# Optimization experiments

Hardware: AMD Instinct MI355X
Metric: run time of the kernel (lower is better)

Reference implementation:

```python
import jax, jax.numpy as jnp
import numpy as np
from jax import lax

TOP_K = 4
ROUTED_SCALING = 1.0
RENORMALIZE = True


def setup_inputs() -> dict:
    key = jax.random.key(0)
    ks = jax.random.split(key, 9)
    H, I, E = 2048, 1024, 16
    s = 0.02
    return {
        "hidden_states": jax.random.normal(ks[0], (2, 1024, H), jnp.float32),
        "gate_w": jax.random.normal(ks[1], (E, H), jnp.float32) * s,
        "expert_bias": jax.random.normal(ks[2], (E,), jnp.float32) * s,
        "w_gate": jax.random.normal(ks[3], (E, I, H), jnp.float32) * s,
        "w_up": jax.random.normal(ks[4], (E, I, H), jnp.float32) * s,
        "w_down": jax.random.normal(ks[5], (E, H, I), jnp.float32) * s,
        "sw_gate": jax.random.normal(ks[6], (I, H), jnp.float32) * s,
        "sw_up": jax.random.normal(ks[7], (I, H), jnp.float32) * s,
        "sw_down": jax.random.normal(ks[8], (H, I), jnp.float32) * s,
    }


def _swiglu_ffn(x, wg, wu, wd):
    # SiluAndMul(gate_up) -> down_proj
    return (jax.nn.silu(x @ wg.T) * (x @ wu.T)) @ wd.T


def reference(hidden_states, gate_w, expert_bias, w_gate, w_up, w_down,
              sw_gate, sw_up, sw_down):
    orig_shape = hidden_states.shape
    H = orig_shape[-1]
    x = hidden_states.reshape(-1, H)            # [T, H]
    T = x.shape[0]

    # --- sigmoid gating with score-correction bias (bias affects selection only) ---
    logits = x.astype(jnp.float32) @ gate_w.T    # [T, E] fp32 router
    scores = jax.nn.sigmoid(logits)
    _, topk_idx = lax.top_k(scores + expert_bias[None, :], TOP_K)   # [T, K]
    topk_w = jnp.take_along_axis(scores, topk_idx, axis=-1)         # raw scores
    if RENORMALIZE:
        topk_w = topk_w / jnp.sum(topk_w, axis=-1, keepdims=True)
    topk_w = topk_w * ROUTED_SCALING

    # scatter top-k weights into dense [T, E] combine matrix
    E = gate_w.shape[0]
    combine = jnp.zeros((T, E), dtype=x.dtype).at[
        jnp.arange(T)[:, None], topk_idx].set(topk_w.astype(x.dtype))

    # --- routed experts: scan over experts, weighted accumulate ---
    def step(acc, ws):
        wg, wu, wd, cw = ws                     # cw: [T] combine weights
        return acc + cw[:, None] * _swiglu_ffn(x, wg, wu, wd), None

    routed, _ = lax.scan(step, jnp.zeros_like(x),
                         (w_gate, w_up, w_down, combine.T))

    # --- shared expert ---
    shared = _swiglu_ffn(x, sw_gate, sw_up, sw_down)

    return (routed + shared).reshape(orig_shape)
```

## Files before the change

kernel.cpp:

```cpp
#include <hip/hip_runtime.h>
#include <hip/hip_bf16.h>
#include <cstdint>

#define TK 2048
#define HD 2048
#define ID 1024
#define NE 16
#define NG 17
#define TOPK 4
#define SLOTS (TK*TOPK)
#define ROWS_ALL (SLOTS+TK)
#define IH (ID*HD)
#define MAXT 96

typedef __attribute__((ext_vector_type(4))) float f32x4;
typedef __attribute__((ext_vector_type(16))) float f32x16;
typedef __attribute__((ext_vector_type(8))) short s16x8;
typedef unsigned short u16;
typedef unsigned long long u64;

__device__ __forceinline__ u16 f2bf(float f){
  union { float f; uint32_t u; } v; v.f = f;
  uint32_t r = v.u + 0x7fffu + ((v.u >> 16) & 1u);
  return (u16)(r >> 16);
}

#define GLD16(g, l) __builtin_amdgcn_global_load_lds( \
    (const __attribute__((address_space(1))) void*)(g), \
    (__attribute__((address_space(3))) void*)(l), 16, 0, 0)

__device__ __forceinline__ int swz(int r){
  return (r & 7) ^ (((r >> 3) & 3) << 1);
}
__device__ __forceinline__ const s16x8* fragp(const u16* b, int row, int off){
  return (const s16x8*)((const char*)b + row*128 + (off ^ (swz(row)<<4)));
}

#define MFMA32(a,b,c) __builtin_amdgcn_mfma_f32_32x32x16_bf16((a),(b),(c),0,0,0)

__global__ void k_prep(const float* __restrict__ x, u16* __restrict__ xb,
                       u64* __restrict__ maskbits, int* __restrict__ tokcnt){
  int gi = blockIdx.x*blockDim.x + threadIdx.x;
  int st = gridDim.x*blockDim.x;
  if (gi < NE*32) maskbits[gi] = 0ull;
  if (gi < TK) tokcnt[gi] = 0;
  for (int i=gi; i<TK*HD/4; i+=st){
    float4 f = ((const float4*)x)[i];
    ushort4 o; o.x=f2bf(f.x); o.y=f2bf(f.y); o.z=f2bf(f.z); o.w=f2bf(f.w);
    ((ushort4*)xb)[i] = o;
  }
}

__global__ void k_cvtw(const float* __restrict__ wg, const float* __restrict__ wu,
                       const float* __restrict__ wd, const float* __restrict__ swg,
                       const float* __restrict__ swu, const float* __restrict__ swd,
                       u16* __restrict__ wgb, u16* __restrict__ wub, u16* __restrict__ wdb){
  const size_t nbig = (size_t)NE*IH/4, nsml = IH/4;
  const size_t total = 3*nbig + 3*nsml;
  for (size_t i = (size_t)blockIdx.x*blockDim.x + threadIdx.x; i < total;
       i += (size_t)gridDim.x*blockDim.x){
    const float4* src; ushort4* dst; size_t j = i;
    if (j < nbig){ src=(const float4*)wg + j;  dst=(ushort4*)wgb + j; }
    else if ((j-=nbig) < nbig){ src=(const float4*)wu + j;  dst=(ushort4*)wub + j; }
    else if ((j-=nbig) < nbig){ src=(const float4*)wd + j;  dst=(ushort4*)wdb + j; }
    else if ((j-=nbig) < nsml){ src=(const float4*)swg + j; dst=(ushort4*)wgb + nbig + j; }
    else if ((j-=nsml) < nsml){ src=(const float4*)swu + j; dst=(ushort4*)wub + nbig + j; }
    else { j-=nsml; src=(const float4*)swd + j; dst=(ushort4*)wdb + nbig + j; }
    float4 f = *src;
    ushort4 o; o.x=f2bf(f.x); o.y=f2bf(f.y); o.z=f2bf(f.z); o.w=f2bf(f.w);
    *dst = o;
  }
}

__global__ __launch_bounds__(256) void k_logits(const float* __restrict__ x,
                                                const float* __restrict__ gw,
                                                const float* __restrict__ bias,
                                                float* __restrict__ wdense,
                                                u64* __restrict__ maskbits){
  int t = blockIdx.x, tid = threadIdx.x;
  int lane = tid & 63, wv = tid >> 6;
  const float* xr = x + (size_t)t*HD;
  float acc[NE];
  #pragma unroll
  for (int e=0;e<NE;e++) acc[e]=0.f;
  for (int k=tid;k<HD;k+=256){
    float xv = xr[k];
    #pragma unroll
    for (int e=0;e<NE;e++) acc[e] += xv * gw[e*HD + k];
  }
  __shared__ float red[NE][4];
  #pragma unroll
  for (int e=0;e<NE;e++){
    float v = acc[e];
    #pragma unroll
    for (int off=32;off>0;off>>=1) v += __shfl_down(v, off, 64);
    if (lane==0) red[e][wv] = v;
  }
  __syncthreads();
  if (tid == 0){
    float sc[NE], bs[NE];
    #pragma unroll
    for (int e=0;e<NE;e++){
      float l = red[e][0]+red[e][1]+red[e][2]+red[e][3];
      float s = 1.f/(1.f+expf(-l));
      sc[e]=s; bs[e]=s+bias[e];
    }
    int idx[TOPK]; float wsum=0.f; unsigned used=0;
    for (int k=0;k<TOPK;k++){
      int best=0; float bv=-1e30f;
      for (int e=0;e<NE;e++) if (!((used>>e)&1u) && bs[e] > bv){ bv=bs[e]; best=e; }
      used |= 1u<<best; idx[k]=best; wsum += sc[best];
    }
    float inv = 1.f/wsum;
    for (int k=0;k<TOPK;k++){
      int e = idx[k];
      wdense[t*NE + e] = sc[e]*inv;
      atomicOr(&maskbits[e*32 + (t>>6)], 1ull << (t&63));
    }
  }
}

__global__ void k_scan(const u64* __restrict__ maskbits, int* __restrict__ counts,
                       int* __restrict__ offsets, int* __restrict__ wordpfx,
                       int* __restrict__ tiles){
  int acc = 0;
  for (int e=0;e<NE;e++){
    int c = 0;
    for (int w=0;w<32;w++){ wordpfx[e*32+w] = c; c += __popcll(maskbits[e*32+w]); }
    counts[e] = c;
  }
  for (int e=0;e<NE;e++){ offsets[e] = acc; acc += counts[e]; }
  offsets[NE] = acc;
  counts[NE] = TK;
  int nt = 0;
  for (int g=0; g<NG; g++){
    int c = counts[g];
    for (int mt=0; mt*128 < c && nt < MAXT; mt++) tiles[nt++] = (g<<8) | mt;
  }
  for (; nt<MAXT; nt++) tiles[nt] = -1;
}

__global__ void k_scatter(const u64* __restrict__ maskbits, const int* __restrict__ offsets,
                          const int* __restrict__ wordpfx, const float* __restrict__ wdense,
                          int* __restrict__ rowtok, float* __restrict__ roww,
                          int* __restrict__ tokcnt, int* __restrict__ tok4){
  int t = blockIdx.x*blockDim.x + threadIdx.x;
  int e = blockIdx.y;
  if (t >= TK) return;
  if (e == NE){ rowtok[offsets[NE]+t] = t; roww[offsets[NE]+t] = 1.f; return; }
  u64 w = maskbits[e*32 + (t>>6)];
  if ((w >> (t&63)) & 1ull){
    int pos = offsets[e] + wordpfx[e*32 + (t>>6)] + __popcll(w & ((1ull << (t&63)) - 1ull));
    rowtok[pos] = t; roww[pos] = wdense[t*NE + e];
    int r = atomicAdd(&tokcnt[t], 1);
    tok4[t*TOPK + r] = pos;
  }
}

__global__ __launch_bounds__(256, 2) void k_gemm1b(
    const u16* __restrict__ xb, const u16* __restrict__ wgb, const u16* __restrict__ wub,
    const int* __restrict__ counts, const int* __restrict__ offsets,
    const int* __restrict__ rowtok, const float* __restrict__ roww,
    const int* __restrict__ tiles, u16* __restrict__ P)
{
  int te = tiles[blockIdx.y];
  if (te < 0) return;
  int g = te >> 8, mt = te & 255;
  int cnt = counts[g];
  int n0 = blockIdx.x*128;
  int base = offsets[g];
  const u16* wg16 = wgb + (size_t)g*IH;
  const u16* wu16 = wub + (size_t)g*IH;

  __shared__ u16 lsA[128*64];
  __shared__ u16 lsG[128*64];
  __shared__ u16 lsU[128*64];

  int tid = threadIdx.x, lane = tid & 63, wv = tid >> 6;
  int wm = (wv>>1)*64, wn64 = (wv&1)*64;
  int rl = lane & 31, hi = lane >> 5;

  f32x16 accg[2][2] = {}; f32x16 accu[2][2] = {};

  const u16 *aSrc[4], *gSrc[4], *uSrc[4];
  #pragma unroll
  for (int i=0;i<4;i++){
    int b = i*256 + tid, r = b>>3, cb = b&7;
    int m = mt*128 + r; if (m >= cnt) m = cnt-1;
    int tok = rowtok[base + m];
    aSrc[i] = xb + (size_t)tok*HD + ((cb ^ swz(r))<<3);
    size_t woff = (size_t)(n0 + r)*HD + ((cb ^ swz(r))<<3);
    gSrc[i] = wg16 + woff; uSrc[i] = wu16 + woff;
  }

  for (int t=0; t<HD/64; ++t){
    int k0 = t*64;
    #pragma unroll
    for (int i=0;i<4;i++) GLD16(aSrc[i]+k0, lsA + (i*256 + wv*64)*8);
    #pragma unroll
    for (int i=0;i<4;i++) GLD16(gSrc[i]+k0, lsG + (i*256 + wv*64)*8);
    #pragma unroll
    for (int i=0;i<4;i++) GLD16(uSrc[i]+k0, lsU + (i*256 + wv*64)*8);
    asm volatile("s_waitcnt vmcnt(0)" ::: "memory");
    __builtin_amdgcn_s_barrier();
    #pragma unroll
    for (int s=0; s<4; ++s){
      int off = s*32 + hi*16;
      s16x8 af[2], bg[2], bu[2];
      af[0] = *fragp(lsA, wm + rl, off);
      af[1] = *fragp(lsA, wm + 32 + rl, off);
      bg[0] = *fragp(lsG, wn64 + rl, off);
      bg[1] = *fragp(lsG, wn64 + 32 + rl, off);
      bu[0] = *fragp(lsU, wn64 + rl, off);
      bu[1] = *fragp(lsU, wn64 + 32 + rl, off);
      #pragma unroll
      for (int mi=0;mi<2;mi++){
        #pragma unroll
        for (int j=0;j<2;j++){
          accg[mi][j] = MFMA32(af[mi], bg[j], accg[mi][j]);
          accu[mi][j] = MFMA32(af[mi], bu[j], accu[mi][j]);
        }
      }
    }
    asm volatile("s_waitcnt lgkmcnt(0)" ::: "memory");
    __builtin_amdgcn_s_barrier();
  }
  #pragma unroll
  for (int mi=0;mi<2;mi++){
    #pragma unroll
    for (int r=0;r<16;r++){
      int rowb = wm + mi*32 + (r&3) + 8*(r>>2) + 4*hi;
      int m = mt*128 + rowb;
      if (m < cnt){
        int slot = base + m;
        float wgt = roww[slot];
        #pragma unroll
        for (int j=0;j<2;j++){
          float gv = accg[mi][j][r], uv = accu[mi][j][r];
          float pv = gv/(1.f+expf(-gv))*uv*wgt;
          P[(size_t)slot*ID + n0 + wn64 + j*32 + rl] = f2bf(pv);
        }
      }
    }
  }
}

__global__ __launch_bounds__(256, 2) void k_gemm2b(
    const u16* __restrict__ P, const u16* __restrict__ wdb,
    const int* __restrict__ counts, const int* __restrict__ offsets,
    const int* __restrict__ tiles, u16* __restrict__ R)
{
  int te = tiles[blockIdx.y];
  if (te < 0) return;
  int g = te >> 8, mt = te & 255;
  int cnt = counts[g];
  int base = offsets[g];
  int n0 = blockIdx.x*256;
  const u16* wd16 = wdb + (size_t)g*IH;

  __shared__ u16 lsA[128*64];
  __shared__ u16 lsB[256*64];

  int tid = threadIdx.x, lane = tid & 63, wv = tid >> 6;
  int wm = (wv>>1)*64, wn = (wv&1)*128;
  int rl = lane & 31, hi = lane >> 5;
  f32x16 acc[2][4] = {};

  const u16* aSrc[4];
  #pragma unroll
  for (int i=0;i<4;i++){
    int b = i*256 + tid, r = b>>3, cb = b&7;
    int m = mt*128 + r; if (m >= cnt) m = cnt-1;
    aSrc[i] = P + (size_t)(base + m)*ID + ((cb ^ swz(r))<<3);
  }
  const u16* bSrc[8];
  #pragma unroll
  for (int i=0;i<8;i++){
    int b = i*256 + tid, r = b>>3, cb = b&7;
    bSrc[i] = wd16 + (size_t)(n0 + r)*ID + ((cb ^ swz(r))<<3);
  }

  for (int t=0; t<ID/64; ++t){
    int k0 = t*64;
    #pragma unroll
    for (int i=0;i<4;i++) GLD16(aSrc[i]+k0, lsA + (i*256 + wv*64)*8);
    #pragma unroll
    for (int i=0;i<8;i++) GLD16(bSrc[i]+k0, lsB + (i*256 + wv*64)*8);
    asm volatile("s_waitcnt vmcnt(0)" ::: "memory");
    __builtin_amdgcn_s_barrier();
    #pragma unroll
    for (int s=0; s<4; ++s){
      int off = s*32 + hi*16;
      s16x8 af[2], bf[4];
      af[0] = *fragp(lsA, wm + rl, off);
      af[1] = *fragp(lsA, wm + 32 + rl, off);
      #pragma unroll
      for (int nj=0;nj<4;nj++) bf[nj] = *fragp(lsB, wn + nj*32 + rl, off);
      #pragma unroll
      for (int mi=0;mi<2;mi++)
        #pragma unroll
        for (int nj=0;nj<4;nj++)
          acc[mi][nj] = MFMA32(af[mi], bf[nj], acc[mi][nj]);
    }
    asm volatile("s_waitcnt lgkmcnt(0)" ::: "memory");
    __builtin_amdgcn_s_barrier();
  }
  #pragma unroll
  for (int mi=0;mi<2;mi++){
    #pragma unroll
    for (int r=0;r<16;r++){
      int rowb = wm + mi*32 + (r&3) + 8*(r>>2) + 4*hi;
      int m = mt*128 + rowb;
      if (m < cnt){
        u16* rrow = R + (size_t)(base + m)*HD + n0 + wn + rl;
        #pragma unroll
        for (int nj=0;nj<4;nj++) rrow[nj*32] = f2bf(acc[mi][nj][r]);
      }
    }
  }
}

__global__ __launch_bounds__(256) void k_reduce(const u16* __restrict__ R,
                                                const int* __restrict__ tok4,
                                                float* __restrict__ out){
  int t = blockIdx.x;
  int c0 = threadIdx.x * 8;
  int s0 = tok4[t*TOPK+0], s1 = tok4[t*TOPK+1], s2 = tok4[t*TOPK+2], s3 = tok4[t*TOPK+3];
  const ushort4* p0 = (const ushort4*)(R + (size_t)s0*HD + c0);
  const ushort4* p1 = (const ushort4*)(R + (size_t)s1*HD + c0);
  const ushort4* p2 = (const ushort4*)(R + (size_t)s2*HD + c0);
  const ushort4* p3 = (const ushort4*)(R + (size_t)s3*HD + c0);
  const ushort4* ps = (const ushort4*)(R + (size_t)(SLOTS + t)*HD + c0);
  float* o = out + (size_t)t*HD + c0;
  #pragma unroll
  for (int h=0; h<2; h++){
    ushort4 a = p0[h], b = p1[h], c = p2[h], d = p3[h], e = ps[h];
    #pragma unroll
    for (int j=0;j<4;j++){
      u16 ua = ((const u16*)&a)[j], ub = ((const u16*)&b)[j];
      u16 uc = ((const u16*)&c)[j], ud = ((const u16*)&d)[j], ue = ((const u16*)&e)[j];
      float v = ((float)(int)0);
      union { uint32_t u; float f; } w;
      w.u = (uint32_t)ua<<16; v  = w.f;
      w.u = (uint32_t)ub<<16; v += w.f;
      w.u = (uint32_t)uc<<16; v += w.f;
      w.u = (uint32_t)ud<<16; v += w.f;
      w.u = (uint32_t)ue<<16; v += w.f;
      o[h*4 + j] = v;
    }
  }
}


extern "C" void kernel_launch(void* const* d_in, const int* in_sizes, int n_in,
                              void* d_out, int out_size, void* d_ws, size_t ws_size,
                              hipStream_t stream){
  (void)in_sizes; (void)n_in; (void)ws_size; (void)out_size;
  const float* x       = (const float*)d_in[0];
  const float* gate_w  = (const float*)d_in[1];
  const float* ebias   = (const float*)d_in[2];
  const float* w_gate  = (const float*)d_in[3];
  const float* w_up    = (const float*)d_in[4];
  const float* w_down  = (const float*)d_in[5];
  const float* sw_gate = (const float*)d_in[6];
  const float* sw_up   = (const float*)d_in[7];
  const float* sw_down = (const float*)d_in[8];
  float* out = (float*)d_out;

  char* p = (char*)d_ws;
  auto alloc = [&](size_t bytes)->char*{ char* r = p; p += (bytes + 255) & ~(size_t)255; return r; };
  u16*   xb       = (u16*)  alloc((size_t)TK*HD*2);
  u16*   P        = (u16*)  alloc((size_t)ROWS_ALL*ID*2);
  float* wdense   = (float*)alloc((size_t)TK*NE*4);
  u64*   maskbits = (u64*)  alloc((size_t)NE*32*8);
  int*   wordpfx  = (int*)  alloc((size_t)NE*32*4);
  int*   counts   = (int*)  alloc(64);
  int*   offsets  = (int*)  alloc(64);
  int*   tiles    = (int*)  alloc(MAXT*4);
  int*   rowtok   = (int*)  alloc((size_t)ROWS_ALL*4);
  float* roww     = (float*)alloc((size_t)ROWS_ALL*4);
  int*   tokcnt   = (int*)  alloc((size_t)TK*4);
  int*   tok4     = (int*)  alloc((size_t)TK*TOPK*4);
  size_t slab = (size_t)NG*IH*2;
  u16* wgb = (u16*)alloc(slab);
  u16* wub = (u16*)alloc(slab);
  u16* wdb = (u16*)alloc(slab);
  u16* R = wgb;

  k_prep<<<2048, 256, 0, stream>>>(x, xb, maskbits, tokcnt);
  k_cvtw<<<2048, 256, 0, stream>>>(w_gate, w_up, w_down, sw_gate, sw_up, sw_down,
                                   wgb, wub, wdb);
  k_logits<<<TK, 256, 0, stream>>>(x, gate_w, ebias, wdense, maskbits);
  k_scan<<<1, 1, 0, stream>>>(maskbits, counts, offsets, wordpfx, tiles);
  k_scatter<<<dim3(TK/256, NG), 256, 0, stream>>>(maskbits, offsets, wordpfx, wdense,
                                                  rowtok, roww, tokcnt, tok4);

  dim3 g1(ID/128, MAXT);
  k_gemm1b<<<g1, 256, 0, stream>>>(xb, wgb, wub, counts, offsets, rowtok, roww, tiles, P);
  dim3 g2(HD/256, MAXT);
  k_gemm2b<<<g2, 256, 0, stream>>>(P, wdb, counts, offsets, tiles, R);
  k_reduce<<<TK, 256, 0, stream>>>(R, tok4, out);
}
```

Before: 393.2 us.

## Interleave gate/up weights, enlarge GEMM tiles to 256x256, double-buffer LDS

Weight conversion now interleaves gate and up rows in blocks of 32 into one buffer, so gemm1 loads a single B tile and computes gate/up pairs within each wave. Both grouped GEMMs move to 512-thread blocks with 256-row M tiles and 256-column N tiles, and they double-buffer LDS with prefetch of the next K slice and raised wave priority around the MFMA loop. The swizzle is simplified to row&7 and the tile count per expert is halved. The aim is more data reuse per block and load latency hidden behind compute. The cost is larger LDS use (128KB) and more padding waste for experts with small token counts.

Measured after the change: 422.8 us. 7.5% more time.

```diff
diff --git a/kernel.cpp b/kernel.cpp
--- a/kernel.cpp
+++ b/kernel.cpp
@@ -11,7 +11,7 @@
 #define SLOTS (TK*TOPK)
 #define ROWS_ALL (SLOTS+TK)
 #define IH (ID*HD)
-#define MAXT 96
+#define MAXT 64
 
 typedef __attribute__((ext_vector_type(4))) float f32x4;
 typedef __attribute__((ext_vector_type(16))) float f32x16;
@@ -29,11 +29,8 @@
     (const __attribute__((address_space(1))) void*)(g), \
     (__attribute__((address_space(3))) void*)(l), 16, 0, 0)
 
-__device__ __forceinline__ int swz(int r){
-  return (r & 7) ^ (((r >> 3) & 3) << 1);
-}
 __device__ __forceinline__ const s16x8* fragp(const u16* b, int row, int off){
-  return (const s16x8*)((const char*)b + row*128 + (off ^ (swz(row)<<4)));
+  return (const s16x8*)((const char*)b + row*128 + (off ^ ((row&7)<<4)));
 }
 
 #define MFMA32(a,b,c) __builtin_amdgcn_mfma_f32_32x32x16_bf16((a),(b),(c),0,0,0)
@@ -54,18 +51,34 @@
 __global__ void k_cvtw(const float* __restrict__ wg, const float* __restrict__ wu,
                        const float* __restrict__ wd, const float* __restrict__ swg,
                        const float* __restrict__ swu, const float* __restrict__ swd,
-                       u16* __restrict__ wgb, u16* __restrict__ wub, u16* __restrict__ wdb){
-  const size_t nbig = (size_t)NE*IH/4, nsml = IH/4;
-  const size_t total = 3*nbig + 3*nsml;
-  for (size_t i = (size_t)blockIdx.x*blockDim.x + threadIdx.x; i < total;
+                       u16* __restrict__ wgu, u16* __restrict__ wdb){
+  const size_t ngu = (size_t)NG*2048*(HD/4);
+  const size_t nd  = (size_t)NG*2048*(ID/4);
+  for (size_t i = (size_t)blockIdx.x*blockDim.x + threadIdx.x; i < ngu + nd;
        i += (size_t)gridDim.x*blockDim.x){
-    const float4* src; ushort4* dst; size_t j = i;
-    if (j < nbig){ src=(const float4*)wg + j;  dst=(ushort4*)wgb + j; }
-    else if ((j-=nbig) < nbig){ src=(const float4*)wu + j;  dst=(ushort4*)wub + j; }
-    else if ((j-=nbig) < nbig){ src=(const float4*)wd + j;  dst=(ushort4*)wdb + j; }
-    else if ((j-=nbig) < nsml){ src=(const float4*)swg + j; dst=(ushort4*)wgb + nbig + j; }
-    else if ((j-=nsml) < nsml){ src=(const float4*)swu + j; dst=(ushort4*)wub + nbig + j; }
-    else { j-=nsml; src=(const float4*)swd + j; dst=(ushort4*)wdb + nbig + j; }
+    const float4* src; ushort4* dst;
+    if (i < ngu){
+      int g   = (int)(i / (2048*(size_t)(HD/4)));
+      int rem = (int)(i % (2048*(size_t)(HD/4)));
+      int J   = rem / (HD/4);
+      int kv  = rem % (HD/4);
+      int rp  = (J>>6)*32 + (J&31);
+      const float* s;
+      if (g < NE) s = ((J&32) ? wu : wg) + (size_t)g*IH + (size_t)rp*HD;
+      else        s = ((J&32) ? swu : swg) + (size_t)rp*HD;
+      src = (const float4*)s + kv;
+      dst = (ushort4*)(wgu + (size_t)g*2048*HD + (size_t)J*HD) + kv;
+    } else {
+      size_t j = i - ngu;
+      int g   = (int)(j / (2048*(size_t)(ID/4)));
+      int rem = (int)(j % (2048*(size_t)(ID/4)));
+      int J   = rem / (ID/4);
+      int kv  = rem % (ID/4);
+      const float* s = (g < NE) ? (wd + (size_t)g*IH + (size_t)J*ID)
+                                : (swd + (size_t)J*ID);
+      src = (const float4*)s + kv;
+      dst = (ushort4*)(wdb + (size_t)g*2048*ID + (size_t)J*ID) + kv;
+    }
     float4 f = *src;
     ushort4 o; o.x=f2bf(f.x); o.y=f2bf(f.y); o.z=f2bf(f.z); o.w=f2bf(f.w);
     *dst = o;
@@ -135,7 +148,7 @@
   int nt = 0;
   for (int g=0; g<NG; g++){
     int c = counts[g];
-    for (int mt=0; mt*128 < c && nt < MAXT; mt++) tiles[nt++] = (g<<8) | mt;
+    for (int mt=0; mt*256 < c && nt < MAXT; mt++) tiles[nt++] = (g<<8) | mt;
   }
   for (; nt<MAXT; nt++) tiles[nt] = -1;
 }
@@ -157,8 +170,8 @@
   }
 }
 
-__global__ __launch_bounds__(256, 2) void k_gemm1b(
-    const u16* __restrict__ xb, const u16* __restrict__ wgb, const u16* __restrict__ wub,
+__global__ __launch_bounds__(512, 2) void k_gemm1b(
+    const u16* __restrict__ xb, const u16* __restrict__ wgu,
     const int* __restrict__ counts, const int* __restrict__ offsets,
     const int* __restrict__ rowtok, const float* __restrict__ roww,
     const int* __restrict__ tiles, u16* __restrict__ P)
@@ -167,85 +180,87 @@
   if (te < 0) return;
   int g = te >> 8, mt = te & 255;
   int cnt = counts[g];
-  int n0 = blockIdx.x*128;
+  int x = blockIdx.x;
   int base = offsets[g];
-  const u16* wg16 = wgb + (size_t)g*IH;
-  const u16* wu16 = wub + (size_t)g*IH;
-
-  __shared__ u16 lsA[128*64];
-  __shared__ u16 lsG[128*64];
-  __shared__ u16 lsU[128*64];
+  const u16* B0 = wgu + (size_t)g*2048*HD + (size_t)(x*256)*HD;
+
+  __shared__ u16 lsA[2][256*64];
+  __shared__ u16 lsB[2][256*64];
 
   int tid = threadIdx.x, lane = tid & 63, wv = tid >> 6;
-  int wm = (wv>>1)*64, wn64 = (wv&1)*64;
+  int wm = (wv>>2)*128, wc = wv & 3;
   int rl = lane & 31, hi = lane >> 5;
 
-  f32x16 accg[2][2] = {}; f32x16 accu[2][2] = {};
-
-  const u16 *aSrc[4], *gSrc[4], *uSrc[4];
+  f32x16 acc[4][2] = {};
+
+  const u16 *aSrc[4], *bSrc[4];
   #pragma unroll
   for (int i=0;i<4;i++){
-    int b = i*256 + tid, r = b>>3, cb = b&7;
-    int m = mt*128 + r; if (m >= cnt) m = cnt-1;
+    int c = i*512 + tid, r = c>>3, cb = c&7;
+    int m = mt*256 + r; if (m >= cnt) m = cnt-1;
     int tok = rowtok[base + m];
-    aSrc[i] = xb + (size_t)tok*HD + ((cb ^ swz(r))<<3);
-    size_t woff = (size_t)(n0 + r)*HD + ((cb ^ swz(r))<<3);
-    gSrc[i] = wg16 + woff; uSrc[i] = wu16 + woff;
-  }
-
-  for (int t=0; t<HD/64; ++t){
-    int k0 = t*64;
-    #pragma unroll
-    for (int i=0;i<4;i++) GLD16(aSrc[i]+k0, lsA + (i*256 + wv*64)*8);
-    #pragma unroll
-    for (int i=0;i<4;i++) GLD16(gSrc[i]+k0, lsG + (i*256 + wv*64)*8);
-    #pragma unroll
-    for (int i=0;i<4;i++) GLD16(uSrc[i]+k0, lsU + (i*256 + wv*64)*8);
-    asm volatile("s_waitcnt vmcnt(0)" ::: "memory");
+    aSrc[i] = xb + (size_t)tok*HD + ((cb ^ (r&7))<<3);
+    bSrc[i] = B0 + (size_t)r*HD + ((cb ^ (r&7))<<3);
+  }
+
+  #pragma unroll
+  for (int i=0;i<4;i++) GLD16(aSrc[i], &lsA[0][(i*512 + wv*64)*8]);
+  #pragma unroll
+  for (int i=0;i<4;i++) GLD16(bSrc[i], &lsB[0][(i*512 + wv*64)*8]);
+
+  const int ntile = HD/64;
+  for (int t=0; t<ntile; ++t){
+    int cur = t & 1, nxt = cur ^ 1;
+    if (t+1 < ntile){
+      int k1 = (t+1)*64;
+      #pragma unroll
+      for (int i=0;i<4;i++) GLD16(aSrc[i]+k1, &lsA[nxt][(i*512 + wv*64)*8]);
+      #pragma unroll
+      for (int i=0;i<4;i++) GLD16(bSrc[i]+k1, &lsB[nxt][(i*512 + wv*64)*8]);
+      asm volatile("s_waitcnt vmcnt(8)" ::: "memory");
+    } else {
+      asm volatile("s_waitcnt vmcnt(0)" ::: "memory");
+    }
     __builtin_amdgcn_s_barrier();
+    const u16* A = lsA[cur]; const u16* B = lsB[cur];
+    __builtin_amdgcn_s_setprio(1);
     #pragma unroll
     for (int s=0; s<4; ++s){
       int off = s*32 + hi*16;
-      s16x8 af[2], bg[2], bu[2];
-      af[0] = *fragp(lsA, wm + rl, off);
-      af[1] = *fragp(lsA, wm + 32 + rl, off);
-      bg[0] = *fragp(lsG, wn64 + rl, off);
-      bg[1] = *fragp(lsG, wn64 + 32 + rl, off);
-      bu[0] = *fragp(lsU, wn64 + rl, off);
-      bu[1] = *fragp(lsU, wn64 + 32 + rl, off);
-      #pragma unroll
-      for (int mi=0;mi<2;mi++){
-        #pragma unroll
-        for (int j=0;j<2;j++){
-          accg[mi][j] = MFMA32(af[mi], bg[j], accg[mi][j]);
-          accu[mi][j] = MFMA32(af[mi], bu[j], accu[mi][j]);
-        }
+      s16x8 af[4], bf[2];
+      #pragma unroll
+      for (int mi=0;mi<4;mi++) af[mi] = *fragp(A, wm + mi*32 + rl, off);
+      bf[0] = *fragp(B, wc*64 + rl, off);
+      bf[1] = *fragp(B, wc*64 + 32 + rl, off);
+      #pragma unroll
+      for (int mi=0;mi<4;mi++){
+        acc[mi][0] = MFMA32(af[mi], bf[0], acc[mi][0]);
+        acc[mi][1] = MFMA32(af[mi], bf[1], acc[mi][1]);
       }
     }
+    __builtin_amdgcn_s_setprio(0);
     asm volatile("s_waitcnt lgkmcnt(0)" ::: "memory");
     __builtin_amdgcn_s_barrier();
   }
-  #pragma unroll
-  for (int mi=0;mi<2;mi++){
+  int pcol = x*128 + wc*32 + rl;
+  #pragma unroll
+  for (int mi=0;mi<4;mi++){
     #pragma unroll
     for (int r=0;r<16;r++){
       int rowb = wm + mi*32 + (r&3) + 8*(r>>2) + 4*hi;
-      int m = mt*128 + rowb;
+      int m = mt*256 + rowb;
       if (m < cnt){
         int slot = base + m;
         float wgt = roww[slot];
-        #pragma unroll
-        for (int j=0;j<2;j++){
-          float gv = accg[mi][j][r], uv = accu[mi][j][r];
-          float pv = gv/(1.f+expf(-gv))*uv*wgt;
-          P[(size_t)slot*ID + n0 + wn64 + j*32 + rl] = f2bf(pv);
-        }
+        float gv = acc[mi][0][r], uv = acc[mi][1][r];
+        float pv = gv/(1.f+expf(-gv))*uv*wgt;
+        P[(size_t)slot*ID + pcol] = f2bf(pv);
       }
     }
   }
 }
 
-__global__ __launch_bounds__(256, 2) void k_gemm2b(
+__global__ __launch_bounds__(512, 2) void k_gemm2b(
     const u16* __restrict__ P, const u16* __restrict__ wdb,
     const int* __restrict__ counts, const int* __restrict__ offsets,
     const int* __restrict__ tiles, u16* __restrict__ R)
@@ -255,66 +270,76 @@
   int g = te >> 8, mt = te & 255;
   int cnt = counts[g];
   int base = offsets[g];
-  int n0 = blockIdx.x*256;
-  const u16* wd16 = wdb + (size_t)g*IH;
-
-  __shared__ u16 lsA[128*64];
-  __shared__ u16 lsB[256*64];
+  int x = blockIdx.x;
+  const u16* B0 = wdb + (size_t)g*2048*ID + (size_t)(x*256)*ID;
+
+  __shared__ u16 lsA[2][256*64];
+  __shared__ u16 lsB[2][256*64];
 
   int tid = threadIdx.x, lane = tid & 63, wv = tid >> 6;
-  int wm = (wv>>1)*64, wn = (wv&1)*128;
+  int wm = (wv>>2)*128, wc = wv & 3;
   int rl = lane & 31, hi = lane >> 5;
-  f32x16 acc[2][4] = {};
-
-  const u16* aSrc[4];
+  f32x16 acc[4][2] = {};
+
+  const u16 *aSrc[4], *bSrc[4];
   #pragma unroll
   for (int i=0;i<4;i++){
-    int b = i*256 + tid, r = b>>3, cb = b&7;
-    int m = mt*128 + r; if (m >= cnt) m = cnt-1;
-    aSrc[i] = P + (size_t)(base + m)*ID + ((cb ^ swz(r))<<3);
-  }
-  const u16* bSrc[8];
-  #pragma unroll
-  for (int i=0;i<8;i++){
-    int b = i*256 + tid, r = b>>3, cb = b&7;
-    bSrc[i] = wd16 + (size_t)(n0 + r)*ID + ((cb ^ swz(r))<<3);
-  }
-
-  for (int t=0; t<ID/64; ++t){
-    int k0 = t*64;
-    #pragma unroll
-    for (int i=0;i<4;i++) GLD16(aSrc[i]+k0, lsA + (i*256 + wv*64)*8);
-    #pragma unroll
-    for (int i=0;i<8;i++) GLD16(bSrc[i]+k0, lsB + (i*256 + wv*64)*8);
-    asm volatile("s_waitcnt vmcnt(0)" ::: "memory");
+    int c = i*512 + tid, r = c>>3, cb = c&7;
+    int m = mt*256 + r; if (m >= cnt) m = cnt-1;
+    aSrc[i] = P + (size_t)(base + m)*ID + ((cb ^ (r&7))<<3);
+    bSrc[i] = B0 + (size_t)r*ID + ((cb ^ (r&7))<<3);
+  }
+
+  #pragma unroll
+  for (int i=0;i<4;i++) GLD16(aSrc[i], &lsA[0][(i*512 + wv*64)*8]);
+  #pragma unroll
+  for (int i=0;i<4;i++) GLD16(bSrc[i], &lsB[0][(i*512 + wv*64)*8]);
+
+  const int ntile = ID/64;
+  for (int t=0; t<ntile; ++t){
+    int cur = t & 1, nxt = cur ^ 1;
+    if (t+1 < ntile){
+      int k1 = (t+1)*64;
+      #pragma unroll
+      for (int i=0;i<4;i++) GLD16(aSrc[i]+k1, &lsA[nxt][(i*512 + wv*64)*8]);
+      #pragma unroll
+      for (int i=0;i<4;i++) GLD16(bSrc[i]+k1, &lsB[nxt][(i*512 + wv*64)*8]);
+      asm volatile("s_waitcnt vmcnt(8)" ::: "memory");
+    } else {
+      asm volatile("s_waitcnt vmcnt(0)" ::: "memory");
+    }
     __builtin_amdgcn_s_barrier();
+    const u16* A = lsA[cur]; const u16* B = lsB[cur];
+    __builtin_amdgcn_s_setprio(1);
     #pragma unroll
     for (int s=0; s<4; ++s){
       int off = s*32 + hi*16;
-      s16x8 af[2], bf[4];
-      af[0] = *fragp(lsA, wm + rl, off);
-      af[1] = *fragp(lsA, wm + 32 + rl, off);
-      #pragma unroll
-      for (int nj=0;nj<4;nj++) bf[nj] = *fragp(lsB, wn + nj*32 + rl, off);
-      #pragma unroll
-      for (int mi=0;mi<2;mi++)
-        #pragma unroll
-        for (int nj=0;nj<4;nj++)
-          acc[mi][nj] = MFMA32(af[mi], bf[nj], acc[mi][nj]);
-    }
+      s16x8 af[4], bf[2];
+      #pragma unroll
+      for (int mi=0;mi<4;mi++) af[mi] = *fragp(A, wm + mi*32 + rl, off);
+      bf[0] = *fragp(B, wc*64 + rl, off);
+      bf[1] = *fragp(B, wc*64 + 32 + rl, off);
+      #pragma unroll
+      for (int mi=0;mi<4;mi++){
+        acc[mi][0] = MFMA32(af[mi], bf[0], acc[mi][0]);
+        acc[mi][1] = MFMA32(af[mi], bf[1], acc[mi][1]);
+      }
+    }
+    __builtin_amdgcn_s_setprio(0);
     asm volatile("s_waitcnt lgkmcnt(0)" ::: "memory");
     __builtin_amdgcn_s_barrier();
   }
   #pragma unroll
-  for (int mi=0;mi<2;mi++){
+  for (int mi=0;mi<4;mi++){
     #pragma unroll
     for (int r=0;r<16;r++){
       int rowb = wm + mi*32 + (r&3) + 8*(r>>2) + 4*hi;
-      int m = mt*128 + rowb;
+      int m = mt*256 + rowb;
       if (m < cnt){
-        u16* rrow = R + (size_t)(base + m)*HD + n0 + wn + rl;
-        #pragma unroll
-        for (int nj=0;nj<4;nj++) rrow[nj*32] = f2bf(acc[mi][nj][r]);
+        int slot = base + m;
+        u16* rrow = R + (size_t)slot*HD + x*256 + wc*64 + rl;
+        rrow[0]  = f2bf(acc[mi][0][r]);
+        rrow[32] = f2bf(acc[mi][1][r]);
       }
     }
   }
@@ -339,8 +364,8 @@
     for (int j=0;j<4;j++){
       u16 ua = ((const u16*)&a)[j], ub = ((const u16*)&b)[j];
       u16 uc = ((const u16*)&c)[j], ud = ((const u16*)&d)[j], ue = ((const u16*)&e)[j];
-      float v = ((float)(int)0);
       union { uint32_t u; float f; } w;
+      float v;
       w.u = (uint32_t)ua<<16; v  = w.f;
       w.u = (uint32_t)ub<<16; v += w.f;
       w.u = (uint32_t)uc<<16; v += w.f;
@@ -381,23 +406,21 @@
   float* roww     = (float*)alloc((size_t)ROWS_ALL*4);
   int*   tokcnt   = (int*)  alloc((size_t)TK*4);
   int*   tok4     = (int*)  alloc((size_t)TK*TOPK*4);
-  size_t slab = (size_t)NG*IH*2;
-  u16* wgb = (u16*)alloc(slab);
-  u16* wub = (u16*)alloc(slab);
-  u16* wdb = (u16*)alloc(slab);
-  u16* R = wgb;
+  u16* wgu = (u16*)alloc((size_t)NG*2048*HD*2);
+  u16* wdb = (u16*)alloc((size_t)NG*2048*ID*2);
+  u16* R = wgu;
 
   k_prep<<<2048, 256, 0, stream>>>(x, xb, maskbits, tokcnt);
   k_cvtw<<<2048, 256, 0, stream>>>(w_gate, w_up, w_down, sw_gate, sw_up, sw_down,
-                                   wgb, wub, wdb);
+                                   wgu, wdb);
   k_logits<<<TK, 256, 0, stream>>>(x, gate_w, ebias, wdense, maskbits);
   k_scan<<<1, 1, 0, stream>>>(maskbits, counts, offsets, wordpfx, tiles);
   k_scatter<<<dim3(TK/256, NG), 256, 0, stream>>>(maskbits, offsets, wordpfx, wdense,
                                                   rowtok, roww, tokcnt, tok4);
 
   dim3 g1(ID/128, MAXT);
-  k_gemm1b<<<g1, 256, 0, stream>>>(xb, wgb, wub, counts, offsets, rowtok, roww, tiles, P);
+  k_gemm1b<<<g1, 512, 0, stream>>>(xb, wgu, counts, offsets, rowtok, roww, tiles, P);
   dim3 g2(HD/256, MAXT);
-  k_gemm2b<<<g2, 256, 0, stream>>>(P, wdb, counts, offsets, tiles, R);
+  k_gemm2b<<<g2, 512, 0, stream>>>(P, wdb, counts, offsets, tiles, R);
   k_reduce<<<TK, 256, 0, stream>>>(R, tok4, out);
 }
```

## Switch grouped GEMMs to 16x16x32 MFMA with narrower gate/up N tile

Applied to the files above, without the earlier changes.

Both grouped expert GEMMs move from 32x32x16 to 16x16x32 bf16 MFMA instructions, which changes the fragment layouts, the accumulator shapes and the epilogue row mapping. The LDS swizzle is simplified to a plain row&7 XOR. The gate/up GEMM N tile is halved to 64, which doubles its grid in x and halves its LDS footprint. The second launch_bounds occupancy hint is dropped, so the compiler may use more registers, especially in gemm2 where the accumulator tile is larger. The aim is better occupancy and parallelism for gemm1, at the cost of rereading the A tile twice as often and of possible LDS bank conflicts from the weaker swizzle.

After: 425.9 us. 1.08x slower.

```diff
diff --git a/kernel.cpp b/kernel.cpp
--- a/kernel.cpp
+++ b/kernel.cpp
@@ -14,7 +14,6 @@
 #define MAXT 96
 
 typedef __attribute__((ext_vector_type(4))) float f32x4;
-typedef __attribute__((ext_vector_type(16))) float f32x16;
 typedef __attribute__((ext_vector_type(8))) short s16x8;
 typedef unsigned short u16;
 typedef unsigned long long u64;
@@ -29,14 +28,11 @@
     (const __attribute__((address_space(1))) void*)(g), \
     (__attribute__((address_space(3))) void*)(l), 16, 0, 0)
 
-__device__ __forceinline__ int swz(int r){
-  return (r & 7) ^ (((r >> 3) & 3) << 1);
-}
 __device__ __forceinline__ const s16x8* fragp(const u16* b, int row, int off){
-  return (const s16x8*)((const char*)b + row*128 + (off ^ (swz(row)<<4)));
-}
-
-#define MFMA32(a,b,c) __builtin_amdgcn_mfma_f32_32x32x16_bf16((a),(b),(c),0,0,0)
+  return (const s16x8*)((const char*)b + row*128 + (off ^ ((row&7)<<4)));
+}
+
+#define MFMA16(a,b,c) __builtin_amdgcn_mfma_f32_16x16x32_bf16((a),(b),(c),0,0,0)
 
 __global__ void k_prep(const float* __restrict__ x, u16* __restrict__ xb,
                        u64* __restrict__ maskbits, int* __restrict__ tokcnt){
@@ -157,7 +153,7 @@
   }
 }
 
-__global__ __launch_bounds__(256, 2) void k_gemm1b(
+__global__ __launch_bounds__(256) void k_gemm1b(
     const u16* __restrict__ xb, const u16* __restrict__ wgb, const u16* __restrict__ wub,
     const int* __restrict__ counts, const int* __restrict__ offsets,
     const int* __restrict__ rowtok, const float* __restrict__ roww,
@@ -167,85 +163,85 @@
   if (te < 0) return;
   int g = te >> 8, mt = te & 255;
   int cnt = counts[g];
-  int n0 = blockIdx.x*128;
+  int n0 = blockIdx.x*64;
   int base = offsets[g];
   const u16* wg16 = wgb + (size_t)g*IH;
   const u16* wu16 = wub + (size_t)g*IH;
 
   __shared__ u16 lsA[128*64];
-  __shared__ u16 lsG[128*64];
-  __shared__ u16 lsU[128*64];
+  __shared__ u16 lsG[64*64];
+  __shared__ u16 lsU[64*64];
 
   int tid = threadIdx.x, lane = tid & 63, wv = tid >> 6;
-  int wm = (wv>>1)*64, wn64 = (wv&1)*64;
-  int rl = lane & 31, hi = lane >> 5;
-
-  f32x16 accg[2][2] = {}; f32x16 accu[2][2] = {};
-
-  const u16 *aSrc[4], *gSrc[4], *uSrc[4];
+  int wm = (wv>>1)*64, wn = (wv&1)*32;
+  int rl = lane & 15, hi = lane >> 4;
+
+  f32x4 accg[4][2] = {}; f32x4 accu[4][2] = {};
+
+  const u16* aSrc[4];
   #pragma unroll
   for (int i=0;i<4;i++){
     int b = i*256 + tid, r = b>>3, cb = b&7;
     int m = mt*128 + r; if (m >= cnt) m = cnt-1;
     int tok = rowtok[base + m];
-    aSrc[i] = xb + (size_t)tok*HD + ((cb ^ swz(r))<<3);
-    size_t woff = (size_t)(n0 + r)*HD + ((cb ^ swz(r))<<3);
-    gSrc[i] = wg16 + woff; uSrc[i] = wu16 + woff;
-  }
-
-  for (int t=0; t<HD/64; ++t){
-    int k0 = t*64;
+    aSrc[i] = xb + (size_t)tok*HD + ((cb ^ (r&7))<<3);
+  }
+  const u16 *gSrc[2], *uSrc[2];
+  #pragma unroll
+  for (int i=0;i<2;i++){
+    int b = i*256 + tid, r = b>>3, cb = b&7;
+    size_t off = (size_t)(n0 + r)*HD + ((cb ^ (r&7))<<3);
+    gSrc[i] = wg16 + off; uSrc[i] = wu16 + off;
+  }
+
+  for (int k0=0; k0<HD; k0+=64){
     #pragma unroll
     for (int i=0;i<4;i++) GLD16(aSrc[i]+k0, lsA + (i*256 + wv*64)*8);
     #pragma unroll
-    for (int i=0;i<4;i++) GLD16(gSrc[i]+k0, lsG + (i*256 + wv*64)*8);
-    #pragma unroll
-    for (int i=0;i<4;i++) GLD16(uSrc[i]+k0, lsU + (i*256 + wv*64)*8);
-    asm volatile("s_waitcnt vmcnt(0)" ::: "memory");
-    __builtin_amdgcn_s_barrier();
-    #pragma unroll
-    for (int s=0; s<4; ++s){
-      int off = s*32 + hi*16;
-      s16x8 af[2], bg[2], bu[2];
-      af[0] = *fragp(lsA, wm + rl, off);
-      af[1] = *fragp(lsA, wm + 32 + rl, off);
-      bg[0] = *fragp(lsG, wn64 + rl, off);
-      bg[1] = *fragp(lsG, wn64 + 32 + rl, off);
-      bu[0] = *fragp(lsU, wn64 + rl, off);
-      bu[1] = *fragp(lsU, wn64 + 32 + rl, off);
-      #pragma unroll
-      for (int mi=0;mi<2;mi++){
+    for (int i=0;i<2;i++) GLD16(gSrc[i]+k0, lsG + (i*256 + wv*64)*8);
+    #pragma unroll
+    for (int i=0;i<2;i++) GLD16(uSrc[i]+k0, lsU + (i*256 + wv*64)*8);
+    __syncthreads();
+    #pragma unroll
+    for (int ks=0; ks<2; ++ks){
+      int off = ks*64 + hi*16;
+      s16x8 af[4];
+      #pragma unroll
+      for (int mi=0;mi<4;mi++) af[mi] = *fragp(lsA, wm+16*mi+rl, off);
+      #pragma unroll
+      for (int ni=0;ni<2;ni++){
+        s16x8 bg = *fragp(lsG, wn+16*ni+rl, off);
+        s16x8 bu = *fragp(lsU, wn+16*ni+rl, off);
         #pragma unroll
-        for (int j=0;j<2;j++){
-          accg[mi][j] = MFMA32(af[mi], bg[j], accg[mi][j]);
-          accu[mi][j] = MFMA32(af[mi], bu[j], accu[mi][j]);
+        for (int mi=0;mi<4;mi++){
+          accg[mi][ni] = MFMA16(af[mi], bg, accg[mi][ni]);
+          accu[mi][ni] = MFMA16(af[mi], bu, accu[mi][ni]);
         }
       }
     }
-    asm volatile("s_waitcnt lgkmcnt(0)" ::: "memory");
-    __builtin_amdgcn_s_barrier();
-  }
-  #pragma unroll
-  for (int mi=0;mi<2;mi++){
-    #pragma unroll
-    for (int r=0;r<16;r++){
-      int rowb = wm + mi*32 + (r&3) + 8*(r>>2) + 4*hi;
-      int m = mt*128 + rowb;
+    __syncthreads();
+  }
+  int rl4 = hi*4, cl = rl;
+  #pragma unroll
+  for (int mi=0;mi<4;mi++){
+    #pragma unroll
+    for (int j=0;j<4;j++){
+      int m = mt*128 + wm + mi*16 + rl4 + j;
       if (m < cnt){
         int slot = base + m;
         float wgt = roww[slot];
         #pragma unroll
-        for (int j=0;j<2;j++){
-          float gv = accg[mi][j][r], uv = accu[mi][j][r];
+        for (int ni=0;ni<2;ni++){
+          float gv = accg[mi][ni][j], uv = accu[mi][ni][j];
           float pv = gv/(1.f+expf(-gv))*uv*wgt;
-          P[(size_t)slot*ID + n0 + wn64 + j*32 + rl] = f2bf(pv);
+          P[(size_t)slot*ID + n0 + wn + ni*16 + cl] = f2bf(pv);
         }
       }
     }
   }
 }
 
-__global__ __launch_bounds__(256, 2) void k_gemm2b(
+__global__ __launch_bounds__(256) void k_gemm2b(
     const u16* __restrict__ P, const u16* __restrict__ wdb,
     const int* __restrict__ counts, const int* __restrict__ offsets,
     const int* __restrict__ tiles, u16* __restrict__ R)
@@ -263,58 +259,55 @@
 
   int tid = threadIdx.x, lane = tid & 63, wv = tid >> 6;
   int wm = (wv>>1)*64, wn = (wv&1)*128;
-  int rl = lane & 31, hi = lane >> 5;
-  f32x16 acc[2][4] = {};
+  int rl = lane & 15, hi = lane >> 4;
+  f32x4 acc[4][8] = {};
 
   const u16* aSrc[4];
   #pragma unroll
   for (int i=0;i<4;i++){
     int b = i*256 + tid, r = b>>3, cb = b&7;
     int m = mt*128 + r; if (m >= cnt) m = cnt-1;
-    aSrc[i] = P + (size_t)(base + m)*ID + ((cb ^ swz(r))<<3);
+    aSrc[i] = P + (size_t)(base + m)*ID + ((cb ^ (r&7))<<3);
   }
   const u16* bSrc[8];
   #pragma unroll
   for (int i=0;i<8;i++){
     int b = i*256 + tid, r = b>>3, cb = b&7;
-    bSrc[i] = wd16 + (size_t)(n0 + r)*ID + ((cb ^ swz(r))<<3);
-  }
-
-  for (int t=0; t<ID/64; ++t){
-    int k0 = t*64;
+    bSrc[i] = wd16 + (size_t)(n0 + r)*ID + ((cb ^ (r&7))<<3);
+  }
+
+  for (int k0=0; k0<ID; k0+=64){
     #pragma unroll
     for (int i=0;i<4;i++) GLD16(aSrc[i]+k0, lsA + (i*256 + wv*64)*8);
     #pragma unroll
     for (int i=0;i<8;i++) GLD16(bSrc[i]+k0, lsB + (i*256 + wv*64)*8);
-    asm volatile("s_waitcnt vmcnt(0)" ::: "memory");
-    __builtin_amdgcn_s_barrier();
-    #pragma unroll
-    for (int s=0; s<4; ++s){
-      int off = s*32 + hi*16;
-      s16x8 af[2], bf[4];
-      af[0] = *fragp(lsA, wm + rl, off);
-      af[1] = *fragp(lsA, wm + 32 + rl, off);
-      #pragma unroll
-      for (int nj=0;nj<4;nj++) bf[nj] = *fragp(lsB, wn + nj*32 + rl, off);
-      #pragma unroll
-      for (int mi=0;mi<2;mi++)
+    __syncthreads();
+    #pragma unroll
+    for (int ks=0; ks<2; ++ks){
+      int off = ks*64 + hi*16;
+      s16x8 af[4], bf[8];
+      #pragma unroll
+      for (int mi=0;mi<4;mi++) af[mi] = *fragp(lsA, wm+16*mi+rl, off);
+      #pragma unroll
+      for (int nj=0;nj<8;nj++) bf[nj] = *fragp(lsB, wn+16*nj+rl, off);
+      #pragma unroll
+      for (int mi=0;mi<4;mi++)
         #pragma unroll
-        for (int nj=0;nj<4;nj++)
-          acc[mi][nj] = MFMA32(af[mi], bf[nj], acc[mi][nj]);
-    }
-    asm volatile("s_waitcnt lgkmcnt(0)" ::: "memory");
-    __builtin_amdgcn_s_barrier();
-  }
-  #pragma unroll
-  for (int mi=0;mi<2;mi++){
-    #pragma unroll
-    for (int r=0;r<16;r++){
-      int rowb = wm + mi*32 + (r&3) + 8*(r>>2) + 4*hi;
-      int m = mt*128 + rowb;
+        for (int nj=0;nj<8;nj++)
+          acc[mi][nj] = MFMA16(af[mi], bf[nj], acc[mi][nj]);
+    }
+    __syncthreads();
+  }
+  #pragma unroll
+  for (int mi=0;mi<4;mi++){
+    #pragma unroll
+    for (int j=0;j<4;j++){
+      int m = mt*128 + wm + mi*16 + hi*4 + j;
       if (m < cnt){
-        u16* rrow = R + (size_t)(base + m)*HD + n0 + wn + rl;
+        int slot = base + m;
+        u16* rrow = R + (size_t)slot*HD + n0 + wn + rl;
         #pragma unroll
-        for (int nj=0;nj<4;nj++) rrow[nj*32] = f2bf(acc[mi][nj][r]);
+        for (int nj=0;nj<8;nj++) rrow[nj*16] = f2bf(acc[mi][nj][j]);
       }
     }
   }
@@ -339,8 +332,8 @@
     for (int j=0;j<4;j++){
       u16 ua = ((const u16*)&a)[j], ub = ((const u16*)&b)[j];
       u16 uc = ((const u16*)&c)[j], ud = ((const u16*)&d)[j], ue = ((const u16*)&e)[j];
-      float v = ((float)(int)0);
       union { uint32_t u; float f; } w;
+      float v;
       w.u = (uint32_t)ua<<16; v  = w.f;
       w.u = (uint32_t)ub<<16; v += w.f;
       w.u = (uint32_t)uc<<16; v += w.f;
@@ -395,7 +388,7 @@
   k_scatter<<<dim3(TK/256, NG), 256, 0, stream>>>(maskbits, offsets, wordpfx, wdense,
                                                   rowtok, roww, tokcnt, tok4);
 
-  dim3 g1(ID/128, MAXT);
+  dim3 g1(ID/64, MAXT);
   k_gemm1b<<<g1, 256, 0, stream>>>(xb, wgb, wub, counts, offsets, rowtok, roww, tiles, P);
   dim3 g2(HD/256, MAXT);
   k_gemm2b<<<g2, 256, 0, stream>>>(P, wdb, counts, offsets, tiles, R);
```
